# Kernel tuning notes

Hardware: AMD Instinct MI355X
Metric: run time of the kernel (lower is better)

## Reference

```python
import jax, jax.numpy as jnp
import numpy as np


def squash(v, axis=-1):
    # scale = |v|^2 / (1+|v|^2) / |v|  (exactly as in the source)
    s2 = jnp.sum(jnp.square(v), axis=axis, keepdims=True)
    scale = s2 / (1.0 + s2) / jnp.sqrt(s2)
    return scale * v


def setup_inputs() -> dict:
    key = jax.random.key(0)
    k1, k2 = jax.random.split(key)
    B, I, P = 64, 2048, 16   # batch, input_num_capsule, input_dim_vector
    J, D = 32, 32            # num_capsule, dim_vector
    inputs = jax.random.normal(k1, (B, I, P), dtype=jnp.float32)
    W = jax.random.normal(k2, (I, J, P, D), dtype=jnp.float32) * 0.1
    bias = jnp.zeros((1, I, J, 1, 1), dtype=jnp.float32)
    return {"inputs": inputs, "W": W, "bias": bias}


def reference(inputs, W, bias):
    # inputs_hat[b,i,j,d] = inputs[b,i,:] @ W[i,j,:,:]
    # (replaces the tf.scan over batch of per-capsule batch_dot)
    inputs_hat = jnp.einsum('bip,ijpd->bijd', inputs, W)

    # In the source while_loop, c = softmax(self.bias, dim=2) is computed from the
    # ORIGINAL bias every iteration (loop-carried b is never read), so all
    # num_routing iterations yield the identical output; compute it once.
    c = jax.nn.softmax(bias[:, :, :, 0, 0], axis=2)          # [1, I, J]
    s = jnp.einsum('bijd,xij->bjd', inputs_hat, c)            # sum over input capsules
    outputs = squash(s, axis=-1)                              # [B, J, D]
    return outputs
```

## Files before the change

kernel.cpp:

```cpp
#include <hip/hip_runtime.h>
#include <hip/hip_bf16.h>
#include <math.h>

#define I_CAP 2048
#define P_DIM 16
#define J_CAP 32
#define D_DIM 32
#define B_SZ  64
#define KCN   32
#define IPB   (I_CAP / KCN)
#define IPW   (IPB / 4)

typedef __attribute__((ext_vector_type(8)))  short short8_t;
typedef __attribute__((ext_vector_type(16))) float f32x16;

__device__ __forceinline__ short f2bf(float f) {
    __hip_bfloat16 h = __float2bfloat16(f);
    return __builtin_bit_cast(short, h);
}

__global__ __launch_bounds__(256) void caps_softmax_k(const float* __restrict__ bias,
                                                      float* __restrict__ c_tab) {
    int tid = blockIdx.x * 256 + threadIdx.x;
    float x = bias[tid];
    float m = x;
#pragma unroll
    for (int k = 16; k >= 1; k >>= 1) m = fmaxf(m, __shfl_xor(m, k));
    float e = expf(x - m);
    float s = e;
#pragma unroll
    for (int k = 16; k >= 1; k >>= 1) s += __shfl_xor(s, k);
    c_tab[tid] = e / s;
}

__global__ __launch_bounds__(256, 2) void caps_main_k(const float* __restrict__ inputs,
                                                      const float* __restrict__ W,
                                                      const float* __restrict__ c_tab,
                                                      float* __restrict__ partial) {
    __shared__ float red[4 * 4096];
    const int t  = threadIdx.x;
    const int l  = t & 63;
    const int wv = t >> 6;

    const int orig = blockIdx.x;
    const int wgid = (orig & 7) * 64 + (orig >> 3);
    const int kc = wgid >> 4;
    const int jp = wgid & 15;
    const int j0 = jp * 2;

    const int g  = l >> 5;
    const int dn = l & 31;

    const int i0 = kc * IPB + wv * IPW;

    const float* wlane  = W + (((size_t)(i0 * J_CAP + j0)) << 9) + g * 256 + dn;
    const float* alane0 = inputs + ((size_t)dn << 15) + (size_t)i0 * 16 + g * 8;
    const float* alane1 = alane0 + ((size_t)32 << 15);
    const float* cp     = c_tab + i0 * J_CAP + j0;

    f32x16 accA0 = {};
    f32x16 accA1 = {};
    f32x16 accB0 = {};
    f32x16 accB1 = {};

#pragma unroll 2
    for (int r = 0; r < IPW; ++r) {
        const float cj0 = cp[r * J_CAP];
        const float cj1 = cp[r * J_CAP + 1];
        float w0buf[8], w1buf[8];
#pragma unroll
        for (int e = 0; e < 8; ++e) {
            w0buf[e] = wlane[(size_t)r * 16384 + e * 32];
            w1buf[e] = wlane[(size_t)r * 16384 + 512 + e * 32];
        }
        float4 a0 = *(const float4*)(alane0 + r * 16);
        float4 a1 = *(const float4*)(alane0 + r * 16 + 4);
        float4 a2 = *(const float4*)(alane1 + r * 16);
        float4 a3 = *(const float4*)(alane1 + r * 16 + 4);

        short8_t bf0, bf1, af0, af1;
#pragma unroll
        for (int e = 0; e < 8; ++e) bf0[e] = f2bf(w0buf[e] * cj0);
#pragma unroll
        for (int e = 0; e < 8; ++e) bf1[e] = f2bf(w1buf[e] * cj1);
        af0[0] = f2bf(a0.x); af0[1] = f2bf(a0.y); af0[2] = f2bf(a0.z); af0[3] = f2bf(a0.w);
        af0[4] = f2bf(a1.x); af0[5] = f2bf(a1.y); af0[6] = f2bf(a1.z); af0[7] = f2bf(a1.w);
        af1[0] = f2bf(a2.x); af1[1] = f2bf(a2.y); af1[2] = f2bf(a2.z); af1[3] = f2bf(a2.w);
        af1[4] = f2bf(a3.x); af1[5] = f2bf(a3.y); af1[6] = f2bf(a3.z); af1[7] = f2bf(a3.w);

        accA0 = __builtin_amdgcn_mfma_f32_32x32x16_bf16(af0, bf0, accA0, 0, 0, 0);
        accA1 = __builtin_amdgcn_mfma_f32_32x32x16_bf16(af1, bf0, accA1, 0, 0, 0);
        accB0 = __builtin_amdgcn_mfma_f32_32x32x16_bf16(af0, bf1, accB0, 0, 0, 0);
        accB1 = __builtin_amdgcn_mfma_f32_32x32x16_bf16(af1, bf1, accB1, 0, 0, 0);
    }

    {
        float* rw = red + wv * 4096;
#pragma unroll
        for (int reg = 0; reg < 16; ++reg) {
            const int b0 = (reg & 3) + 8 * (reg >> 2) + 4 * g;
            rw[b0 * 32 + dn]               = accA0[reg];
            rw[(b0 + 32) * 32 + dn]        = accA1[reg];
            rw[2048 + b0 * 32 + dn]        = accB0[reg];
            rw[2048 + (b0 + 32) * 32 + dn] = accB1[reg];
        }
    }
    __syncthreads();
    {
        float* dstbase = partial + (size_t)(kc * J_CAP + j0) * 2048;
#pragma unroll
        for (int jj = 0; jj < 2; ++jj) {
#pragma unroll
            for (int s = 0; s < 2; ++s) {
                const int o = jj * 2048 + s * 1024 + t * 4;
                float4 v0 = *(const float4*)(red + o);
                float4 v1 = *(const float4*)(red + 4096 + o);
                float4 v2 = *(const float4*)(red + 8192 + o);
                float4 v3 = *(const float4*)(red + 12288 + o);
                float4 sum = {v0.x + v1.x + v2.x + v3.x,
                              v0.y + v1.y + v2.y + v3.y,
                              v0.z + v1.z + v2.z + v3.z,
                              v0.w + v1.w + v2.w + v3.w};
                *(float4*)(dstbase + o) = sum;
            }
        }
    }
}

__global__ __launch_bounds__(256) void caps_reduce_squash_k(const float* __restrict__ partial,
                                                            float* __restrict__ out) {
    const int t  = threadIdx.x;
    const int j  = blockIdx.x >> 3;
    const int bg = blockIdx.x & 7;
    const int b  = bg * 8 + (t >> 5);
    const int d  = t & 31;

    const float* src = partial + (size_t)j * 2048 + (size_t)b * 32 + d;
    float v = 0.f;
#pragma unroll 4
    for (int kc = 0; kc < KCN; ++kc)
        v += src[(size_t)kc * J_CAP * 2048];

    float sq = v * v;
#pragma unroll
    for (int k = 16; k >= 1; k >>= 1) sq += __shfl_xor(sq, k);
    float scale = sq / (1.0f + sq) / sqrtf(sq);
    out[(size_t)b * (J_CAP * D_DIM) + j * D_DIM + d] = v * scale;
}

extern "C" void kernel_launch(void* const* d_in, const int* in_sizes, int n_in,
                              void* d_out, int out_size, void* d_ws, size_t ws_size,
                              hipStream_t stream) {
    const float* inputs = (const float*)d_in[0];
    const float* W      = (const float*)d_in[1];
    const float* bias   = (const float*)d_in[2];
    float* out = (float*)d_out;

    float* c_tab   = (float*)d_ws;
    float* partial = c_tab + I_CAP * J_CAP;

    caps_softmax_k<<<dim3(256), dim3(256), 0, stream>>>(bias, c_tab);
    caps_main_k<<<dim3(KCN * 16), dim3(256), 0, stream>>>(inputs, W, c_tab, partial);
    caps_reduce_squash_k<<<dim3(256), dim3(256), 0, stream>>>(partial, out);
}
```

Baseline: 39.00 us.

## Fuse bias softmax into main kernel and vectorize reduce-squash kernel

Removes the separate softmax launch: each main-kernel block computes the softmax over its 64 input capsules from bias and keeps the two coefficients it needs in LDS. The main loop unroll grows from 2 to 4. The reduce/squash kernel switches to float4 loads, with two lanes splitting the 32 k-chunks and combining through a shuffle, and launches half as many blocks. This saves a kernel launch and a global round trip for the coefficient table, at the cost of redundant softmax work in every block and an extra barrier before the main loop.

Result: slower. 39.92 us (+2.4%).

```diff
diff --git a/kernel.cpp b/kernel.cpp
--- a/kernel.cpp
+++ b/kernel.cpp
@@ -19,25 +19,12 @@
     return __builtin_bit_cast(short, h);
 }
 
-__global__ __launch_bounds__(256) void caps_softmax_k(const float* __restrict__ bias,
-                                                      float* __restrict__ c_tab) {
-    int tid = blockIdx.x * 256 + threadIdx.x;
-    float x = bias[tid];
-    float m = x;
-#pragma unroll
-    for (int k = 16; k >= 1; k >>= 1) m = fmaxf(m, __shfl_xor(m, k));
-    float e = expf(x - m);
-    float s = e;
-#pragma unroll
-    for (int k = 16; k >= 1; k >>= 1) s += __shfl_xor(s, k);
-    c_tab[tid] = e / s;
-}
-
 __global__ __launch_bounds__(256, 2) void caps_main_k(const float* __restrict__ inputs,
                                                       const float* __restrict__ W,
-                                                      const float* __restrict__ c_tab,
+                                                      const float* __restrict__ bias,
                                                       float* __restrict__ partial) {
     __shared__ float red[4 * 4096];
+    __shared__ float c_lds[64][2];
     const int t  = threadIdx.x;
     const int l  = t & 63;
     const int wv = t >> 6;
@@ -51,22 +38,43 @@
     const int g  = l >> 5;
     const int dn = l & 31;
 
-    const int i0 = kc * IPB + wv * IPW;
+    const int i0blk = kc * IPB;
+    const int i0    = i0blk + wv * IPW;
+
+    {
+        const int jj = t & 31;
+        const int ib = t >> 5;
+#pragma unroll
+        for (int pass = 0; pass < 8; ++pass) {
+            const int ii = pass * 8 + ib;
+            float x = bias[(i0blk + ii) * J_CAP + jj];
+            float m = x;
+#pragma unroll
+            for (int k = 16; k >= 1; k >>= 1) m = fmaxf(m, __shfl_xor(m, k));
+            float e = expf(x - m);
+            float s = e;
+#pragma unroll
+            for (int k = 16; k >= 1; k >>= 1) s += __shfl_xor(s, k);
+            float cv = e / s;
+            if (jj == j0)     c_lds[ii][0] = cv;
+            if (jj == j0 + 1) c_lds[ii][1] = cv;
+        }
+    }
+    __syncthreads();
 
     const float* wlane  = W + (((size_t)(i0 * J_CAP + j0)) << 9) + g * 256 + dn;
     const float* alane0 = inputs + ((size_t)dn << 15) + (size_t)i0 * 16 + g * 8;
     const float* alane1 = alane0 + ((size_t)32 << 15);
-    const float* cp     = c_tab + i0 * J_CAP + j0;
 
     f32x16 accA0 = {};
     f32x16 accA1 = {};
     f32x16 accB0 = {};
     f32x16 accB1 = {};
 
-#pragma unroll 2
+#pragma unroll 4
     for (int r = 0; r < IPW; ++r) {
-        const float cj0 = cp[r * J_CAP];
-        const float cj1 = cp[r * J_CAP + 1];
+        const float cj0 = c_lds[wv * IPW + r][0];
+        const float cj1 = c_lds[wv * IPW + r][1];
         float w0buf[8], w1buf[8];
 #pragma unroll
         for (int e = 0; e < 8; ++e) {
@@ -129,23 +137,31 @@
 
 __global__ __launch_bounds__(256) void caps_reduce_squash_k(const float* __restrict__ partial,
                                                             float* __restrict__ out) {
-    const int t  = threadIdx.x;
-    const int j  = blockIdx.x >> 3;
-    const int bg = blockIdx.x & 7;
-    const int b  = bg * 8 + (t >> 5);
-    const int d  = t & 31;
+    const int tid2 = blockIdx.x * 256 + threadIdx.x;
+    const int row  = tid2 >> 4;
+    const int sub  = tid2 & 15;
+    const int d4   = sub >> 1;
+    const int half = sub & 1;
+    const int j = row >> 6, b = row & 63;
 
-    const float* src = partial + (size_t)j * 2048 + (size_t)b * 32 + d;
-    float v = 0.f;
-#pragma unroll 4
-    for (int kc = 0; kc < KCN; ++kc)
-        v += src[(size_t)kc * J_CAP * 2048];
+    const float* src = partial + ((size_t)(half * 16) * J_CAP + j) * 2048 + b * 32 + d4 * 4;
+    float4 v = {0.f, 0.f, 0.f, 0.f};
+#pragma unroll
+    for (int kc = 0; kc < 16; ++kc) {
+        float4 p = *(const float4*)(src + (size_t)kc * J_CAP * 2048);
+        v.x += p.x; v.y += p.y; v.z += p.z; v.w += p.w;
+    }
+    v.x += __shfl_xor(v.x, 1); v.y += __shfl_xor(v.y, 1);
+    v.z += __shfl_xor(v.z, 1); v.w += __shfl_xor(v.w, 1);
 
-    float sq = v * v;
+    float sq = v.x * v.x + v.y * v.y + v.z * v.z + v.w * v.w;
 #pragma unroll
-    for (int k = 16; k >= 1; k >>= 1) sq += __shfl_xor(sq, k);
+    for (int m = 2; m <= 8; m <<= 1) sq += __shfl_xor(sq, m);
     float scale = sq / (1.0f + sq) / sqrtf(sq);
-    out[(size_t)b * (J_CAP * D_DIM) + j * D_DIM + d] = v * scale;
+    if (half == 0) {
+        float4 o = {v.x * scale, v.y * scale, v.z * scale, v.w * scale};
+        *(float4*)(out + (size_t)b * (J_CAP * D_DIM) + j * D_DIM + d4 * 4) = o;
+    }
 }
 
 extern "C" void kernel_launch(void* const* d_in, const int* in_sizes, int n_in,
@@ -156,10 +172,8 @@
     const float* bias   = (const float*)d_in[2];
     float* out = (float*)d_out;
 
-    float* c_tab   = (float*)d_ws;
-    float* partial = c_tab + I_CAP * J_CAP;
+    float* partial = (float*)d_ws;
 
-    caps_softmax_k<<<dim3(256), dim3(256), 0, stream>>>(bias, c_tab);
-    caps_main_k<<<dim3(KCN * 16), dim3(256), 0, stream>>>(inputs, W, c_tab, partial);
-    caps_reduce_squash_k<<<dim3(256), dim3(256), 0, stream>>>(partial, out);
+    caps_main_k<<<dim3(KCN * 16), dim3(256), 0, stream>>>(inputs, W, bias, partial);
+    caps_reduce_squash_k<<<dim3(128), dim3(256), 0, stream>>>(partial, out);
 }
```
